# Performance work log

Hardware: AMD Instinct MI355X
Metric: run time of the kernel (lower is better)

The kernel has to match this reference:

```python
import jax, jax.numpy as jnp
import numpy as np

N_NODES = 100000
N_REL = 8
N_EDGES = 1_600_000
ED = 64   # entity_dim
RD = 64   # relation_dim
H = 4     # attention heads
A = 16    # attention dim per head
D1, D2 = 32, 16  # conv_dim_list


def _leaky(x):
    return jax.nn.leaky_relu(x, 0.01)  # nn.LeakyReLU default slope


def _l2norm(x):
    n = jnp.sqrt(jnp.sum(x * x, axis=1, keepdims=True))
    return x / jnp.maximum(n, 1e-12)  # F.normalize(p=2, dim=1)


def setup_inputs() -> dict:
    key = jax.random.key(0)
    ks = jax.random.split(key, 16)
    s = 0.1
    return dict(
        src=jax.random.randint(ks[0], (N_EDGES,), 0, N_NODES),
        dst=jax.random.randint(ks[1], (N_EDGES,), 0, N_NODES),
        etype=jax.random.randint(ks[2], (N_EDGES,), 0, N_REL),
        node_ids=jnp.arange(N_NODES),
        user_ids=jax.random.randint(ks[3], (1000,), 0, N_NODES),
        item_ids=jax.random.randint(ks[4], (4096,), 0, N_NODES),
        entity_embed=jax.random.normal(ks[5], (N_NODES, ED)) * s,
        rel_embed=jax.random.normal(ks[6], (N_REL, RD)) * s,
        W_R=jax.random.normal(ks[7], (N_REL, ED, RD)) * s,
        W_A=jax.random.normal(ks[8], (RD, H, A)) * s,
        W1_0=jax.random.normal(ks[9], (ED, D1 // H)) * s,
        b1_0=jnp.zeros((D1 // H,)),
        W2_0=jax.random.normal(ks[10], (ED, D1 // H)) * s,
        b2_0=jnp.zeros((D1 // H,)),
        W1_1=jax.random.normal(ks[11], (D1, D2 // H)) * s,
        b1_1=jnp.zeros((D2 // H,)),
        W2_1=jax.random.normal(ks[12], (D1, D2 // H)) * s,
        b2_1=jnp.zeros((D2 // H,)),
    )


def _compute_attention(entity_embed, rel_embed, W_R, W_A, src, dst, etype):
    # relation-specific edge attention: tanh(e_src W_r W_A) * tanh(e_dst W_r W_A + r W_A)
    WA_flat = W_A.reshape(RD, H * A)
    W_ra = jnp.einsum('rij,jk->rik', W_R, WA_flat)          # [R, ED, H*A]
    proj = jnp.einsum('ne,rek->rnk', entity_embed, W_ra)    # [R, N, H*A]
    r_emb_a = rel_embed @ WA_flat                           # [R, H*A]
    r_mul_t = jnp.tanh(proj[etype, src])                    # [E, H*A]
    r_mul_h = jnp.tanh(proj[etype, dst] + r_emb_a[etype])   # [E, H*A]
    att = (r_mul_t * r_mul_h).reshape(-1, H, A).sum(-1)     # [E, H]
    # edge softmax over incoming edges of each dst node, per head
    m = jax.ops.segment_max(att, dst, num_segments=N_NODES)
    m = jnp.where(jnp.isfinite(m), m, 0.0)
    e = jnp.exp(att - m[dst])
    z = jax.ops.segment_sum(e, dst, num_segments=N_NODES)
    return e / jnp.maximum(z[dst], 1e-12)                   # [E, H]


def _bi_layer(ego, att, src, dst, W1, b1, W2, b2, out_dim):
    # u_mul_e + sum: message = node[src] (broadcast over heads) * att[:, :, None]
    in_dim = ego.shape[1]
    msg = ego[src][:, None, :] * att[:, :, None]            # [E, H, in]
    N_h = jax.ops.segment_sum(msg, dst, num_segments=N_NODES)  # [N, H, in]
    node = ego[:, None, :]                                  # [N, 1, in]
    out1 = _leaky((node + N_h).reshape(-1, in_dim) @ W1 + b1).reshape(N_NODES, out_dim)
    out2 = _leaky((node * N_h).reshape(-1, in_dim) @ W2 + b2).reshape(N_NODES, out_dim)
    return out1 + out2  # dropout p=0 (eval)


def reference(src, dst, etype, node_ids, user_ids, item_ids,
              entity_embed, rel_embed, W_R, W_A,
              W1_0, b1_0, W2_0, b2_0, W1_1, b1_1, W2_1, b2_1):
    att = _compute_attention(entity_embed, rel_embed, W_R, W_A, src, dst, etype)
    ego = entity_embed[node_ids]
    ego1 = _bi_layer(ego, att, src, dst, W1_0, b1_0, W2_0, b2_0, D1)
    ego2 = _bi_layer(ego1, att, src, dst, W1_1, b1_1, W2_1, b2_1, D2)
    all_embed = jnp.concatenate([ego, _l2norm(ego1), _l2norm(ego2)], axis=1)  # [N, 112]
    return all_embed[user_ids] @ all_embed[item_ids].T     # [1000, 4096]
```

## Files before the change

kernel.cpp:

```cpp
#include <hip/hip_runtime.h>
#include <hip/hip_bf16.h>
#include <math.h>

#define NN 100000
#define NR 8
#define NE 1600000

typedef __attribute__((ext_vector_type(8))) short short8v;
typedef __attribute__((ext_vector_type(4))) float float4v;
typedef __attribute__((ext_vector_type(2))) float float2v;

__device__ inline float bf2f(unsigned short u) {
  union { unsigned int i; float f; } v; v.i = ((unsigned int)u) << 16; return v.f;
}
__device__ inline unsigned short f2bf(float f) {
  __hip_bfloat16 h = __float2bfloat16(f);
  return *reinterpret_cast<unsigned short*>(&h);
}
__device__ inline float fast_tanh(float x) {
  float ex = __expf(2.f * x);
  return 1.f - 2.f * __builtin_amdgcn_rcpf(ex + 1.f);
}
__device__ inline unsigned char f2fp8(float f) {
  unsigned int p = __builtin_amdgcn_cvt_pk_fp8_f32(f, f, 0, false);
  return (unsigned char)(p & 0xff);
}

__global__ void k_prep(const float* __restrict__ W_R, const float* __restrict__ W_A,
                       const float* __restrict__ rel, unsigned short* __restrict__ Wbf,
                       float* __restrict__ r_emb_a) {
  int tid = blockIdx.x * 256 + threadIdx.x;
  if (tid < NR * 64 * 64) {
    int r = tid >> 12;
    int i = (tid >> 6) & 63;
    int k = tid & 63;
    float acc = 0.f;
    const float* wr = W_R + (r * 64 + i) * 64;
    for (int j = 0; j < 64; ++j) acc += wr[j] * W_A[j * 64 + k];
    Wbf[(r * 64 + k) * 64 + i] = f2bf(acc);
  } else if (tid < NR * 64 * 64 + NR * 64) {
    int idx = tid - NR * 64 * 64;
    int r = idx >> 6, k = idx & 63;
    float acc = 0.f;
    for (int j = 0; j < 64; ++j) acc += rel[r * 64 + j] * W_A[j * 64 + k];
    r_emb_a[idx] = acc;
  }
}

__global__ void k_cvt(const float* __restrict__ E, unsigned short* __restrict__ Ebf) {
  int i = blockIdx.x * 256 + threadIdx.x;
  float4 v = ((const float4*)E)[i];
  ushort4 o;
  o.x = f2bf(v.x); o.y = f2bf(v.y); o.z = f2bf(v.z); o.w = f2bf(v.w);
  ((ushort4*)Ebf)[i] = o;
}

__global__ void k_proj(const unsigned short* __restrict__ Ebf,
                       const unsigned short* __restrict__ Wbf,
                       const float* __restrict__ rea,
                       unsigned char* __restrict__ T1, unsigned char* __restrict__ T2) {
  int wv = threadIdx.x >> 6, lane = threadIdx.x & 63;
  int n0 = blockIdx.x * 64 + wv * 16;
  int mrow = lane & 15, kg = lane >> 4;
  int nodeA = n0 + mrow;
  if (nodeA >= NN) nodeA = NN - 1;
  const short8v a0 = *(const short8v*)(Ebf + (long)nodeA * 64 + kg * 8);
  const short8v a1 = *(const short8v*)(Ebf + (long)nodeA * 64 + 32 + kg * 8);
  int orow = kg * 4;
  for (int ct = 0; ct < 32; ++ct) {
    int c = ct * 16 + mrow;
    const short8v b0 = *(const short8v*)(Wbf + c * 64 + kg * 8);
    const short8v b1 = *(const short8v*)(Wbf + c * 64 + 32 + kg * 8);
    float4v acc = {0.f, 0.f, 0.f, 0.f};
    acc = __builtin_amdgcn_mfma_f32_16x16x32_bf16(a0, b0, acc, 0, 0, 0);
    acc = __builtin_amdgcn_mfma_f32_16x16x32_bf16(a1, b1, acc, 0, 0, 0);
    float rv = rea[c];
    int r = c >> 6, kk = c & 63;
#pragma unroll
    for (int i = 0; i < 4; ++i) {
      int nd = n0 + orow + i;
      if (nd < NN) {
        long base = ((long)r * NN + nd) * 64 + kk;
        T1[base] = f2fp8(fast_tanh(acc[i]));
        T2[base] = f2fp8(fast_tanh(acc[i] + rv));
      }
    }
  }
}

__global__ void k_hist(const int* __restrict__ dst, int* __restrict__ cnt) {
  int e = blockIdx.x * 256 + threadIdx.x;
  if (e < NE) atomicAdd(&cnt[dst[e]], 1);
}

#define SCAN_B 1024
#define NSCAN ((NN + SCAN_B - 1) / SCAN_B)

__global__ void k_scan1(const int* __restrict__ cnt, int* __restrict__ rowp,
                        int* __restrict__ bsum) {
  __shared__ int s[SCAN_B];
  int t = threadIdx.x, g = blockIdx.x * SCAN_B + t;
  s[t] = (g < NN) ? cnt[g] : 0;
  __syncthreads();
  for (int off = 1; off < SCAN_B; off <<= 1) {
    int x = (t >= off) ? s[t - off] : 0;
    __syncthreads();
    s[t] += x;
    __syncthreads();
  }
  if (g < NN) rowp[g + 1] = s[t];
  if (t == SCAN_B - 1) bsum[blockIdx.x] = s[t];
}

__global__ void k_scan2(int* bsum) {
  if (threadIdx.x == 0) {
    int acc = 0;
    for (int i = 0; i < NSCAN; ++i) { int v = bsum[i]; bsum[i] = acc; acc += v; }
  }
}

__global__ void k_scan3(int* rowp, const int* __restrict__ bsum) {
  int t = threadIdx.x, g = blockIdx.x * SCAN_B + t;
  if (g < NN) rowp[g + 1] += bsum[blockIdx.x];
  if (g == 0) rowp[0] = 0;
}

__global__ void k_scatter(const int* __restrict__ src, const int* __restrict__ dst,
                          const int* __restrict__ etype, const int* __restrict__ rowp,
                          int* __restrict__ cur, uint2* __restrict__ rec) {
  int e = blockIdx.x * 256 + threadIdx.x;
  if (e >= NE) return;
  int d = dst[e];
  int p = rowp[d] + atomicAdd(&cur[d], 1);
  uint2 rv;
  rv.x = ((unsigned int)src[e] << 3) | (unsigned int)etype[e];
  rv.y = (unsigned int)d;
  rec[p] = rv;
}

__global__ void k_att(const unsigned char* __restrict__ T1,
                      const unsigned char* __restrict__ T2,
                      const uint2* __restrict__ rec, int* __restrict__ srcs,
                      float* __restrict__ att) {
  int gid = blockIdx.x * 256 + threadIdx.x;
  int e = gid >> 2;
  int h = gid & 3;
  if (e >= NE) return;
  uint2 rv = rec[e];
  int r = rv.x & 7;
  int s = rv.x >> 3;
  int d = (int)rv.y;
  const uint4 av = *(const uint4*)(T1 + ((long)r * NN + s) * 64 + h * 16);
  const uint4 bv = *(const uint4*)(T2 + ((long)r * NN + d) * 64 + h * 16);
  const unsigned int* ap = (const unsigned int*)&av;
  const unsigned int* bp = (const unsigned int*)&bv;
  float acc = 0.f;
#pragma unroll
  for (int i = 0; i < 4; ++i) {
    float2v a0 = __builtin_amdgcn_cvt_pk_f32_fp8(ap[i], false);
    float2v a1 = __builtin_amdgcn_cvt_pk_f32_fp8(ap[i], true);
    float2v b0 = __builtin_amdgcn_cvt_pk_f32_fp8(bp[i], false);
    float2v b1 = __builtin_amdgcn_cvt_pk_f32_fp8(bp[i], true);
    acc += a0.x * b0.x + a0.y * b0.y + a1.x * b1.x + a1.y * b1.y;
  }
  att[gid] = acc;
  if (h == 0) srcs[e] = s;
}

__global__ void k_softmax(const int* __restrict__ rowp, float* __restrict__ att) {
  int n = (blockIdx.x * 256 + threadIdx.x) >> 6;
  int lane = threadIdx.x & 63;
  if (n >= NN) return;
  int i0 = rowp[n] * 4, i1 = rowp[n + 1] * 4;
  float m = -3.4e38f;
  for (int i = i0 + lane; i < i1; i += 64) m = fmaxf(m, att[i]);
  m = fmaxf(m, __shfl_xor(m, 4));
  m = fmaxf(m, __shfl_xor(m, 8));
  m = fmaxf(m, __shfl_xor(m, 16));
  m = fmaxf(m, __shfl_xor(m, 32));
  float z = 0.f;
  for (int i = i0 + lane; i < i1; i += 64) z += __expf(att[i] - m);
  z += __shfl_xor(z, 4);
  z += __shfl_xor(z, 8);
  z += __shfl_xor(z, 16);
  z += __shfl_xor(z, 32);
  float inv = 1.f / fmaxf(z, 1e-12f);
  for (int i = i0 + lane; i < i1; i += 64) att[i] = __expf(att[i] - m) * inv;
}

__global__ void k_fused0(const float* __restrict__ E, const unsigned short* __restrict__ Ebf,
                         const float* __restrict__ attn,
                         const int* __restrict__ rowp, const int* __restrict__ srcs,
                         const float* __restrict__ W1, const float* __restrict__ b1,
                         const float* __restrict__ W2, const float* __restrict__ b2,
                         float* __restrict__ ego1, unsigned short* __restrict__ ego1bf) {
  __shared__ float wt1[8][68], wt2[8][68];
  __shared__ float bb[16];
  __shared__ float s1[4][4][68], s2[4][4][68];
  int t = threadIdx.x;
  for (int i = t; i < 512; i += 256) {
    int d = i >> 3, j = i & 7;
    wt1[j][d] = W1[i];
    wt2[j][d] = W2[i];
  }
  if (t < 8) bb[t] = b1[t];
  else if (t < 16) bb[t] = b2[t - 8];
  __syncthreads();
  int wv = t >> 6, lane = t & 63;
  int n = blockIdx.x * 4 + wv;
  int p0 = rowp[n], p1 = rowp[n + 1];
  int g = lane >> 4, q = lane & 15;
  float acc[4][4];
#pragma unroll
  for (int h = 0; h < 4; ++h)
#pragma unroll
    for (int j = 0; j < 4; ++j) acc[h][j] = 0.f;
  for (int p = p0 + g; p < p1; p += 4) {
    int s = srcs[p];
    float4 a = ((const float4*)attn)[p];
    ushort4 ev = *(const ushort4*)(Ebf + s * 64 + q * 4);
    float e0 = bf2f(ev.x), e1 = bf2f(ev.y), e2 = bf2f(ev.z), e3 = bf2f(ev.w);
    acc[0][0] += a.x * e0; acc[0][1] += a.x * e1; acc[0][2] += a.x * e2; acc[0][3] += a.x * e3;
    acc[1][0] += a.y * e0; acc[1][1] += a.y * e1; acc[1][2] += a.y * e2; acc[1][3] += a.y * e3;
    acc[2][0] += a.z * e0; acc[2][1] += a.z * e1; acc[2][2] += a.z * e2; acc[2][3] += a.z * e3;
    acc[3][0] += a.w * e0; acc[3][1] += a.w * e1; acc[3][2] += a.w * e2; acc[3][3] += a.w * e3;
  }
#pragma unroll
  for (int h = 0; h < 4; ++h)
#pragma unroll
    for (int j = 0; j < 4; ++j) {
      acc[h][j] += __shfl_xor(acc[h][j], 16);
      acc[h][j] += __shfl_xor(acc[h][j], 32);
    }
  if (lane < 16) {
    float4 edv = *(const float4*)(E + n * 64 + q * 4);
#pragma unroll
    for (int h = 0; h < 4; ++h) {
      float4 v1, v2;
      v1.x = edv.x + acc[h][0]; v2.x = edv.x * acc[h][0];
      v1.y = edv.y + acc[h][1]; v2.y = edv.y * acc[h][1];
      v1.z = edv.z + acc[h][2]; v2.z = edv.z * acc[h][2];
      v1.w = edv.w + acc[h][3]; v2.w = edv.w * acc[h][3];
      *(float4*)&s1[wv][h][q * 4] = v1;
      *(float4*)&s2[wv][h][q * 4] = v2;
    }
  }
  __syncthreads();
  int h = (lane >> 3) & 3, j = lane & 7;
  const float* sp = (lane < 32) ? &s1[wv][h][0] : &s2[wv][h][0];
  const float* wp = (lane < 32) ? &wt1[j][0] : &wt2[j][0];
  float o = 0.f;
#pragma unroll
  for (int d = 0; d < 64; d += 4) {
    float4 sv = *(const float4*)(sp + d);
    float4 wv4 = *(const float4*)(wp + d);
    o += sv.x * wv4.x + sv.y * wv4.y + sv.z * wv4.z + sv.w * wv4.w;
  }
  o += (lane < 32) ? bb[j] : bb[8 + j];
  o = (o >= 0.f) ? o : 0.01f * o;
  float other = __shfl_xor(o, 32);
  if (lane < 32) {
    float r = o + other;
    ego1[n * 32 + h * 8 + j] = r;
    ego1bf[n * 32 + h * 8 + j] = f2bf(r);
  }
}

__global__ void k_fused1(const float* __restrict__ ego1, const unsigned short* __restrict__ E1bf,
                         const float* __restrict__ attn,
                         const int* __restrict__ rowp, const int* __restrict__ srcs,
                         const float* __restrict__ W1, const float* __restrict__ b1,
                         const float* __restrict__ W2, const float* __restrict__ b2,
                         float* __restrict__ ego2) {
  __shared__ float wt1[4][36], wt2[4][36], bb[8];
  __shared__ float s1[4][4][36], s2[4][4][36];
  int t = threadIdx.x;
  if (t < 128) { int d = t >> 2, j = t & 3; wt1[j][d] = W1[t]; wt2[j][d] = W2[t]; }
  if (t < 4) bb[t] = b1[t];
  else if (t < 8) bb[t] = b2[t - 4];
  __syncthreads();
  int wv = t >> 6, lane = t & 63;
  int n = blockIdx.x * 4 + wv;
  int p0 = rowp[n], p1 = rowp[n + 1];
  int g = lane >> 3, q = lane & 7;
  float acc[4][4];
#pragma unroll
  for (int h = 0; h < 4; ++h)
#pragma unroll
    for (int j = 0; j < 4; ++j) acc[h][j] = 0.f;
  for (int p = p0 + g; p < p1; p += 8) {
    int s = srcs[p];
    float4 a = ((const float4*)attn)[p];
    ushort4 ev = *(const ushort4*)(E1bf + s * 32 + q * 4);
    float e0 = bf2f(ev.x), e1 = bf2f(ev.y), e2 = bf2f(ev.z), e3 = bf2f(ev.w);
    acc[0][0] += a.x * e0; acc[0][1] += a.x * e1; acc[0][2] += a.x * e2; acc[0][3] += a.x * e3;
    acc[1][0] += a.y * e0; acc[1][1] += a.y * e1; acc[1][2] += a.y * e2; acc[1][3] += a.y * e3;
    acc[2][0] += a.z * e0; acc[2][1] += a.z * e1; acc[2][2] += a.z * e2; acc[2][3] += a.z * e3;
    acc[3][0] += a.w * e0; acc[3][1] += a.w * e1; acc[3][2] += a.w * e2; acc[3][3] += a.w * e3;
  }
#pragma unroll
  for (int h = 0; h < 4; ++h)
#pragma unroll
    for (int j = 0; j < 4; ++j) {
      acc[h][j] += __shfl_xor(acc[h][j], 8);
      acc[h][j] += __shfl_xor(acc[h][j], 16);
      acc[h][j] += __shfl_xor(acc[h][j], 32);
    }
  if (lane < 8) {
    float4 e1v = *(const float4*)(ego1 + n * 32 + q * 4);
#pragma unroll
    for (int h = 0; h < 4; ++h) {
      float4 v1, v2;
      v1.x = e1v.x + acc[h][0]; v2.x = e1v.x * acc[h][0];
      v1.y = e1v.y + acc[h][1]; v2.y = e1v.y * acc[h][1];
      v1.z = e1v.z + acc[h][2]; v2.z = e1v.z * acc[h][2];
      v1.w = e1v.w + acc[h][3]; v2.w = e1v.w * acc[h][3];
      *(float4*)&s1[wv][h][q * 4] = v1;
      *(float4*)&s2[wv][h][q * 4] = v2;
    }
  }
  __syncthreads();
  if (lane < 32) {
    int h = (lane >> 2) & 3, j = lane & 3;
    const float* sp = (lane < 16) ? &s1[wv][h][0] : &s2[wv][h][0];
    const float* wp = (lane < 16) ? &wt1[j][0] : &wt2[j][0];
    float o = 0.f;
#pragma unroll
    for (int d = 0; d < 32; d += 4) {
      float4 sv = *(const float4*)(sp + d);
      float4 wv4 = *(const float4*)(wp + d);
      o += sv.x * wv4.x + sv.y * wv4.y + sv.z * wv4.z + sv.w * wv4.w;
    }
    o += (lane < 16) ? bb[j] : bb[4 + j];
    o = (o >= 0.f) ? o : 0.01f * o;
    float other = __shfl_xor(o, 16);
    if (lane < 16) ego2[n * 16 + h * 4 + j] = o + other;
  }
}

__global__ void k_uv(const float* __restrict__ E, const float* __restrict__ E1,
                     const float* __restrict__ E2, const int* __restrict__ uid,
                     const int* __restrict__ iid, float* __restrict__ U,
                     float* __restrict__ V) {
  int row = (blockIdx.x * 256 + threadIdx.x) >> 6;
  int lane = threadIdx.x & 63;
  if (row >= 1000 + 4096) return;
  int id = (row < 1000) ? uid[row] : iid[row - 1000];
  float* dest = (row < 1000) ? (U + row * 112) : (V + (row - 1000) * 112);
  float v1 = (lane < 32) ? E1[id * 32 + lane] : 0.f;
  float s1 = v1 * v1;
  for (int m = 1; m < 64; m <<= 1) s1 += __shfl_xor(s1, m);
  float v2 = (lane < 16) ? E2[id * 16 + lane] : 0.f;
  float s2 = v2 * v2;
  for (int m = 1; m < 64; m <<= 1) s2 += __shfl_xor(s2, m);
  float i1 = 1.f / fmaxf(sqrtf(s1), 1e-12f);
  float i2 = 1.f / fmaxf(sqrtf(s2), 1e-12f);
  dest[lane] = E[id * 64 + lane];
  if (lane < 32) dest[64 + lane] = v1 * i1;
  if (lane < 16) dest[96 + lane] = v2 * i2;
}

__global__ void k_gemm(const float* __restrict__ U, const float* __restrict__ V,
                       float* __restrict__ C) {
  __shared__ float Us[16][113], Vs[16][113];
  int tx = threadIdx.x & 15, ty = threadIdx.x >> 4;
  int u0 = blockIdx.y * 16, v0 = blockIdx.x * 16;
  for (int i = threadIdx.x; i < 16 * 112; i += 256) {
    int rr = i / 112, cc = i % 112;
    int ur = u0 + rr;
    Us[rr][cc] = (ur < 1000) ? U[ur * 112 + cc] : 0.f;
    Vs[rr][cc] = V[(v0 + rr) * 112 + cc];
  }
  __syncthreads();
  int u = u0 + ty;
  if (u >= 1000) return;
  float acc = 0.f;
#pragma unroll
  for (int k = 0; k < 112; ++k) acc += Us[ty][k] * Vs[tx][k];
  C[u * 4096 + v0 + tx] = acc;
}

extern "C" void kernel_launch(void* const* d_in, const int* in_sizes, int n_in,
                              void* d_out, int out_size, void* d_ws, size_t ws_size,
                              hipStream_t stream) {
  const int* src = (const int*)d_in[0];
  const int* dst = (const int*)d_in[1];
  const int* etype = (const int*)d_in[2];
  const int* uid = (const int*)d_in[4];
  const int* iid = (const int*)d_in[5];
  const float* entity = (const float*)d_in[6];
  const float* rel = (const float*)d_in[7];
  const float* W_R = (const float*)d_in[8];
  const float* W_A = (const float*)d_in[9];
  const float* W1_0 = (const float*)d_in[10];
  const float* b1_0 = (const float*)d_in[11];
  const float* W2_0 = (const float*)d_in[12];
  const float* b2_0 = (const float*)d_in[13];
  const float* W1_1 = (const float*)d_in[14];
  const float* b1_1 = (const float*)d_in[15];
  const float* W2_1 = (const float*)d_in[16];
  const float* b2_1 = (const float*)d_in[17];
  float* out = (float*)d_out;

  char* ws = (char*)d_ws;
  unsigned char*  T1   = (unsigned char*) (ws + 0);
  float*          ego1 = (float*)         (ws + 0);
  unsigned short* e1bf = (unsigned short*)(ws + 12800000);
  float*          ego2 = (float*)         (ws + 19200000);
  float*          U    = (float*)         (ws + 25600000);
  float*          V    = (float*)         (ws + 26048000);
  unsigned char*  T2   = (unsigned char*) (ws + 51200000);
  float*          att  = (float*)         (ws + 102400000);
  uint2*          rec  = (uint2*)         (ws + 128000000);
  int*            srcs = (int*)           (ws + 140800000);
  int*            rowp = (int*)           (ws + 147200000);
  int*            cnt  = (int*)           (ws + 147600128);
  int*            bsum = (int*)           (ws + 148000256);
  unsigned short* Wbf  = (unsigned short*)(ws + 148000768);
  float*          rea  = (float*)         (ws + 148066304);
  unsigned short* Ebf  = (unsigned short*)(ws + 148068352);

  hipMemsetAsync(cnt, 0, NN * sizeof(int), stream);
  k_prep<<<130, 256, 0, stream>>>(W_R, W_A, rel, Wbf, rea);
  k_cvt<<<6250, 256, 0, stream>>>(entity, Ebf);
  k_proj<<<(NN + 63) / 64, 256, 0, stream>>>(Ebf, Wbf, rea, T1, T2);
  k_hist<<<NE / 256, 256, 0, stream>>>(dst, cnt);
  k_scan1<<<NSCAN, SCAN_B, 0, stream>>>(cnt, rowp, bsum);
  k_scan2<<<1, 64, 0, stream>>>(bsum);
  k_scan3<<<NSCAN, SCAN_B, 0, stream>>>(rowp, bsum);
  hipMemsetAsync(cnt, 0, NN * sizeof(int), stream);
  k_scatter<<<NE / 256, 256, 0, stream>>>(src, dst, etype, rowp, cnt, rec);
  k_att<<<NE * 4 / 256, 256, 0, stream>>>(T1, T2, rec, srcs, att);
  k_softmax<<<NN / 4, 256, 0, stream>>>(rowp, att);
  k_fused0<<<NN / 4, 256, 0, stream>>>(entity, Ebf, att, rowp, srcs,
                                       W1_0, b1_0, W2_0, b2_0, ego1, e1bf);
  k_fused1<<<NN / 4, 256, 0, stream>>>(ego1, e1bf, att, rowp, srcs,
                                       W1_1, b1_1, W2_1, b2_1, ego2);
  k_uv<<<(1000 + 4096 + 3) / 4, 256, 0, stream>>>(entity, ego1, ego2, uid, iid, U, V);
  k_gemm<<<dim3(4096 / 16, (1000 + 15) / 16), 256, 0, stream>>>(U, V, out);
}
```

Measured before the change: 610.2 us.

## Fuse edge attention and softmax into layer-0 aggregation with node-major projections

Removes the separate attention and softmax kernels by computing per-edge attention scores inside k_fused0. It uses unnormalized exp weights and applies the per-head reciprocal sum at the end. The projection tables are relaid out node-major ([N][512]) so that one wave reads a contiguous 64-byte row per edge. Edge records shrink to 4 bytes, and layer 1 reuses the stored exp weights with the saved normalizers. Dropping the max subtraction risks overflow for large scores. The layer-0 loop now handles edges one at a time with shuffle reductions, which serializes work per node.

New measurement: 695.0 us. 1.14x slower.

```diff
diff --git a/kernel.cpp b/kernel.cpp
--- a/kernel.cpp
+++ b/kernel.cpp
@@ -24,6 +24,10 @@
 __device__ inline unsigned char f2fp8(float f) {
   unsigned int p = __builtin_amdgcn_cvt_pk_fp8_f32(f, f, 0, false);
   return (unsigned char)(p & 0xff);
+}
+__device__ inline float fp82f(unsigned char b) {
+  float2v v = __builtin_amdgcn_cvt_pk_f32_fp8((unsigned int)b, false);
+  return v.x;
 }
 
 __global__ void k_prep(const float* __restrict__ W_R, const float* __restrict__ W_A,
@@ -58,7 +62,7 @@
 __global__ void k_proj(const unsigned short* __restrict__ Ebf,
                        const unsigned short* __restrict__ Wbf,
                        const float* __restrict__ rea,
-                       unsigned char* __restrict__ T1, unsigned char* __restrict__ T2) {
+                       unsigned char* __restrict__ T1n, unsigned char* __restrict__ T2n) {
   int wv = threadIdx.x >> 6, lane = threadIdx.x & 63;
   int n0 = blockIdx.x * 64 + wv * 16;
   int mrow = lane & 15, kg = lane >> 4;
@@ -75,14 +79,13 @@
     acc = __builtin_amdgcn_mfma_f32_16x16x32_bf16(a0, b0, acc, 0, 0, 0);
     acc = __builtin_amdgcn_mfma_f32_16x16x32_bf16(a1, b1, acc, 0, 0, 0);
     float rv = rea[c];
-    int r = c >> 6, kk = c & 63;
 #pragma unroll
     for (int i = 0; i < 4; ++i) {
       int nd = n0 + orow + i;
       if (nd < NN) {
-        long base = ((long)r * NN + nd) * 64 + kk;
-        T1[base] = f2fp8(fast_tanh(acc[i]));
-        T2[base] = f2fp8(fast_tanh(acc[i] + rv));
+        long base = (long)nd * 512 + c;
+        T1n[base] = f2fp8(fast_tanh(acc[i]));
+        T2n[base] = f2fp8(fast_tanh(acc[i] + rv));
       }
     }
   }
@@ -127,70 +130,20 @@
 
 __global__ void k_scatter(const int* __restrict__ src, const int* __restrict__ dst,
                           const int* __restrict__ etype, const int* __restrict__ rowp,
-                          int* __restrict__ cur, uint2* __restrict__ rec) {
+                          int* __restrict__ cur, unsigned int* __restrict__ rec) {
   int e = blockIdx.x * 256 + threadIdx.x;
   if (e >= NE) return;
   int d = dst[e];
   int p = rowp[d] + atomicAdd(&cur[d], 1);
-  uint2 rv;
-  rv.x = ((unsigned int)src[e] << 3) | (unsigned int)etype[e];
-  rv.y = (unsigned int)d;
-  rec[p] = rv;
-}
-
-__global__ void k_att(const unsigned char* __restrict__ T1,
-                      const unsigned char* __restrict__ T2,
-                      const uint2* __restrict__ rec, int* __restrict__ srcs,
-                      float* __restrict__ att) {
-  int gid = blockIdx.x * 256 + threadIdx.x;
-  int e = gid >> 2;
-  int h = gid & 3;
-  if (e >= NE) return;
-  uint2 rv = rec[e];
-  int r = rv.x & 7;
-  int s = rv.x >> 3;
-  int d = (int)rv.y;
-  const uint4 av = *(const uint4*)(T1 + ((long)r * NN + s) * 64 + h * 16);
-  const uint4 bv = *(const uint4*)(T2 + ((long)r * NN + d) * 64 + h * 16);
-  const unsigned int* ap = (const unsigned int*)&av;
-  const unsigned int* bp = (const unsigned int*)&bv;
-  float acc = 0.f;
-#pragma unroll
-  for (int i = 0; i < 4; ++i) {
-    float2v a0 = __builtin_amdgcn_cvt_pk_f32_fp8(ap[i], false);
-    float2v a1 = __builtin_amdgcn_cvt_pk_f32_fp8(ap[i], true);
-    float2v b0 = __builtin_amdgcn_cvt_pk_f32_fp8(bp[i], false);
-    float2v b1 = __builtin_amdgcn_cvt_pk_f32_fp8(bp[i], true);
-    acc += a0.x * b0.x + a0.y * b0.y + a1.x * b1.x + a1.y * b1.y;
-  }
-  att[gid] = acc;
-  if (h == 0) srcs[e] = s;
-}
-
-__global__ void k_softmax(const int* __restrict__ rowp, float* __restrict__ att) {
-  int n = (blockIdx.x * 256 + threadIdx.x) >> 6;
-  int lane = threadIdx.x & 63;
-  if (n >= NN) return;
-  int i0 = rowp[n] * 4, i1 = rowp[n + 1] * 4;
-  float m = -3.4e38f;
-  for (int i = i0 + lane; i < i1; i += 64) m = fmaxf(m, att[i]);
-  m = fmaxf(m, __shfl_xor(m, 4));
-  m = fmaxf(m, __shfl_xor(m, 8));
-  m = fmaxf(m, __shfl_xor(m, 16));
-  m = fmaxf(m, __shfl_xor(m, 32));
-  float z = 0.f;
-  for (int i = i0 + lane; i < i1; i += 64) z += __expf(att[i] - m);
-  z += __shfl_xor(z, 4);
-  z += __shfl_xor(z, 8);
-  z += __shfl_xor(z, 16);
-  z += __shfl_xor(z, 32);
-  float inv = 1.f / fmaxf(z, 1e-12f);
-  for (int i = i0 + lane; i < i1; i += 64) att[i] = __expf(att[i] - m) * inv;
+  rec[p] = ((unsigned int)src[e] << 3) | (unsigned int)etype[e];
 }
 
 __global__ void k_fused0(const float* __restrict__ E, const unsigned short* __restrict__ Ebf,
-                         const float* __restrict__ attn,
-                         const int* __restrict__ rowp, const int* __restrict__ srcs,
+                         const unsigned char* __restrict__ T1n,
+                         const unsigned char* __restrict__ T2n,
+                         const unsigned int* __restrict__ rec,
+                         const int* __restrict__ rowp,
+                         float* __restrict__ att4, float* __restrict__ zinv4,
                          const float* __restrict__ W1, const float* __restrict__ b1,
                          const float* __restrict__ W2, const float* __restrict__ b2,
                          float* __restrict__ ego1, unsigned short* __restrict__ ego1bf) {
@@ -209,42 +162,51 @@
   int wv = t >> 6, lane = t & 63;
   int n = blockIdx.x * 4 + wv;
   int p0 = rowp[n], p1 = rowp[n + 1];
-  int g = lane >> 4, q = lane & 15;
-  float acc[4][4];
-#pragma unroll
-  for (int h = 0; h < 4; ++h)
-#pragma unroll
-    for (int j = 0; j < 4; ++j) acc[h][j] = 0.f;
-  for (int p = p0 + g; p < p1; p += 4) {
-    int s = srcs[p];
-    float4 a = ((const float4*)attn)[p];
-    ushort4 ev = *(const ushort4*)(Ebf + s * 64 + q * 4);
-    float e0 = bf2f(ev.x), e1 = bf2f(ev.y), e2 = bf2f(ev.z), e3 = bf2f(ev.w);
-    acc[0][0] += a.x * e0; acc[0][1] += a.x * e1; acc[0][2] += a.x * e2; acc[0][3] += a.x * e3;
-    acc[1][0] += a.y * e0; acc[1][1] += a.y * e1; acc[1][2] += a.y * e2; acc[1][3] += a.y * e3;
-    acc[2][0] += a.z * e0; acc[2][1] += a.z * e1; acc[2][2] += a.z * e2; acc[2][3] += a.z * e3;
-    acc[3][0] += a.w * e0; acc[3][1] += a.w * e1; acc[3][2] += a.w * e2; acc[3][3] += a.w * e3;
-  }
-#pragma unroll
-  for (int h = 0; h < 4; ++h)
-#pragma unroll
-    for (int j = 0; j < 4; ++j) {
-      acc[h][j] += __shfl_xor(acc[h][j], 16);
-      acc[h][j] += __shfl_xor(acc[h][j], 32);
-    }
-  if (lane < 16) {
-    float4 edv = *(const float4*)(E + n * 64 + q * 4);
-#pragma unroll
-    for (int h = 0; h < 4; ++h) {
-      float4 v1, v2;
-      v1.x = edv.x + acc[h][0]; v2.x = edv.x * acc[h][0];
-      v1.y = edv.y + acc[h][1]; v2.y = edv.y * acc[h][1];
-      v1.z = edv.z + acc[h][2]; v2.z = edv.z * acc[h][2];
-      v1.w = edv.w + acc[h][3]; v2.w = edv.w * acc[h][3];
-      *(float4*)&s1[wv][h][q * 4] = v1;
-      *(float4*)&s2[wv][h][q * 4] = v2;
-    }
-  }
+  int head = lane >> 4, base = lane & 15;
+  float acc0 = 0.f, acc1 = 0.f, acc2 = 0.f, acc3 = 0.f, z = 0.f;
+  if (p0 < p1) {
+    unsigned int rv = rec[p0];
+    int s = rv >> 3, r = rv & 7;
+    unsigned char a8 = T1n[(long)s * 512 + r * 64 + lane];
+    unsigned char b8 = T2n[(long)n * 512 + r * 64 + lane];
+    unsigned short ev16 = Ebf[s * 64 + lane];
+    for (int p = p0; p < p1; ++p) {
+      int pn = (p + 1 < p1) ? p + 1 : p;
+      unsigned int rvn = rec[pn];
+      int sn = rvn >> 3, rn = rvn & 7;
+      unsigned char a8n = T1n[(long)sn * 512 + rn * 64 + lane];
+      unsigned char b8n = T2n[(long)n * 512 + rn * 64 + lane];
+      unsigned short evn = Ebf[sn * 64 + lane];
+      float a = fp82f(a8), b = fp82f(b8);
+      float prod = a * b;
+      prod += __shfl_xor(prod, 1);
+      prod += __shfl_xor(prod, 2);
+      prod += __shfl_xor(prod, 4);
+      prod += __shfl_xor(prod, 8);
+      float e = __expf(prod);
+      z += e;
+      float w0 = __shfl(e, base);
+      float w1 = __shfl(e, 16 + base);
+      float w2 = __shfl(e, 32 + base);
+      float w3 = __shfl(e, 48 + base);
+      if (lane == 0) ((float4*)att4)[p] = make_float4(w0, w1, w2, w3);
+      float ev = bf2f(ev16);
+      acc0 += w0 * ev; acc1 += w1 * ev; acc2 += w2 * ev; acc3 += w3 * ev;
+      a8 = a8n; b8 = b8n; ev16 = evn;
+    }
+  }
+  float zi = 1.f / fmaxf(z, 1e-12f);
+  if (base == 0) zinv4[n * 4 + head] = zi;
+  float zi0 = __shfl(zi, base);
+  float zi1 = __shfl(zi, 16 + base);
+  float zi2 = __shfl(zi, 32 + base);
+  float zi3 = __shfl(zi, 48 + base);
+  acc0 *= zi0; acc1 *= zi1; acc2 *= zi2; acc3 *= zi3;
+  float ed = E[n * 64 + lane];
+  s1[wv][0][lane] = ed + acc0; s2[wv][0][lane] = ed * acc0;
+  s1[wv][1][lane] = ed + acc1; s2[wv][1][lane] = ed * acc1;
+  s1[wv][2][lane] = ed + acc2; s2[wv][2][lane] = ed * acc2;
+  s1[wv][3][lane] = ed + acc3; s2[wv][3][lane] = ed * acc3;
   __syncthreads();
   int h = (lane >> 3) & 3, j = lane & 7;
   const float* sp = (lane < 32) ? &s1[wv][h][0] : &s2[wv][h][0];
@@ -267,8 +229,9 @@
 }
 
 __global__ void k_fused1(const float* __restrict__ ego1, const unsigned short* __restrict__ E1bf,
-                         const float* __restrict__ attn,
-                         const int* __restrict__ rowp, const int* __restrict__ srcs,
+                         const float* __restrict__ att4, const float* __restrict__ zinv4,
+                         const unsigned int* __restrict__ rec,
+                         const int* __restrict__ rowp,
                          const float* __restrict__ W1, const float* __restrict__ b1,
                          const float* __restrict__ W2, const float* __restrict__ b2,
                          float* __restrict__ ego2) {
@@ -289,8 +252,8 @@
 #pragma unroll
     for (int j = 0; j < 4; ++j) acc[h][j] = 0.f;
   for (int p = p0 + g; p < p1; p += 8) {
-    int s = srcs[p];
-    float4 a = ((const float4*)attn)[p];
+    int s = (int)(rec[p] >> 3);
+    float4 a = ((const float4*)att4)[p];
     ushort4 ev = *(const ushort4*)(E1bf + s * 32 + q * 4);
     float e0 = bf2f(ev.x), e1 = bf2f(ev.y), e2 = bf2f(ev.z), e3 = bf2f(ev.w);
     acc[0][0] += a.x * e0; acc[0][1] += a.x * e1; acc[0][2] += a.x * e2; acc[0][3] += a.x * e3;
@@ -307,6 +270,11 @@
       acc[h][j] += __shfl_xor(acc[h][j], 32);
     }
   if (lane < 8) {
+    float4 zi = *(const float4*)(zinv4 + n * 4);
+#pragma unroll
+    for (int j = 0; j < 4; ++j) {
+      acc[0][j] *= zi.x; acc[1][j] *= zi.y; acc[2][j] *= zi.z; acc[3][j] *= zi.w;
+    }
     float4 e1v = *(const float4*)(ego1 + n * 32 + q * 4);
 #pragma unroll
     for (int h = 0; h < 4; ++h) {
@@ -403,38 +371,37 @@
   float* out = (float*)d_out;
 
   char* ws = (char*)d_ws;
-  unsigned char*  T1   = (unsigned char*) (ws + 0);
-  float*          ego1 = (float*)         (ws + 0);
-  unsigned short* e1bf = (unsigned short*)(ws + 12800000);
-  float*          ego2 = (float*)         (ws + 19200000);
-  float*          U    = (float*)         (ws + 25600000);
-  float*          V    = (float*)         (ws + 26048000);
-  unsigned char*  T2   = (unsigned char*) (ws + 51200000);
-  float*          att  = (float*)         (ws + 102400000);
-  uint2*          rec  = (uint2*)         (ws + 128000000);
-  int*            srcs = (int*)           (ws + 140800000);
-  int*            rowp = (int*)           (ws + 147200000);
-  int*            cnt  = (int*)           (ws + 147600128);
-  int*            bsum = (int*)           (ws + 148000256);
-  unsigned short* Wbf  = (unsigned short*)(ws + 148000768);
-  float*          rea  = (float*)         (ws + 148066304);
-  unsigned short* Ebf  = (unsigned short*)(ws + 148068352);
+  unsigned char*  T1n  = (unsigned char*) (ws + 0);
+  unsigned char*  T2n  = (unsigned char*) (ws + 51200000);
+  float*          att4 = (float*)         (ws + 102400000);
+  unsigned int*   rec  = (unsigned int*)  (ws + 128000000);
+  int*            rowp = (int*)           (ws + 134400000);
+  int*            cnt  = (int*)           (ws + 134800128);
+  int*            bsum = (int*)           (ws + 135200256);
+  unsigned short* Wbf  = (unsigned short*)(ws + 135200768);
+  float*          rea  = (float*)         (ws + 135266304);
+  unsigned short* Ebf  = (unsigned short*)(ws + 135268352);
+  float*          zinv4= (float*)         (ws + 148068352);
+  float*          ego1 = (float*)         (ws + 149668352);
+  unsigned short* e1bf = (unsigned short*)(ws + 162468352);
+  float*          ego2 = (float*)         (ws + 168868352);
+  float*          U    = (float*)         (ws + 175268352);
+  float*          V    = (float*)         (ws + 175716352);
 
   hipMemsetAsync(cnt, 0, NN * sizeof(int), stream);
   k_prep<<<130, 256, 0, stream>>>(W_R, W_A, rel, Wbf, rea);
   k_cvt<<<6250, 256, 0, stream>>>(entity, Ebf);
-  k_proj<<<(NN + 63) / 64, 256, 0, stream>>>(Ebf, Wbf, rea, T1, T2);
+  k_proj<<<(NN + 63) / 64, 256, 0, stream>>>(Ebf, Wbf, rea, T1n, T2n);
   k_hist<<<NE / 256, 256, 0, stream>>>(dst, cnt);
   k_scan1<<<NSCAN, SCAN_B, 0, stream>>>(cnt, rowp, bsum);
   k_scan2<<<1, 64, 0, stream>>>(bsum);
   k_scan3<<<NSCAN, SCAN_B, 0, stream>>>(rowp, bsum);
   hipMemsetAsync(cnt, 0, NN * sizeof(int), stream);
   k_scatter<<<NE / 256, 256, 0, stream>>>(src, dst, etype, rowp, cnt, rec);
-  k_att<<<NE * 4 / 256, 256, 0, stream>>>(T1, T2, rec, srcs, att);
-  k_softmax<<<NN / 4, 256, 0, stream>>>(rowp, att);
-  k_fused0<<<NN / 4, 256, 0, stream>>>(entity, Ebf, att, rowp, srcs,
-                                       W1_0, b1_0, W2_0, b2_0, ego1, e1bf);
-  k_fused1<<<NN / 4, 256, 0, stream>>>(ego1, e1bf, att, rowp, srcs,
+  k_fused0<<<NN / 4, 256, 0, stream>>>(entity, Ebf, T1n, T2n, rec, rowp,
+                                       att4, zinv4, W1_0, b1_0, W2_0, b2_0,
+                                       ego1, e1bf);
+  k_fused1<<<NN / 4, 256, 0, stream>>>(ego1, e1bf, att4, zinv4, rec, rowp,
                                        W1_1, b1_1, W2_1, b2_1, ego2);
   k_uv<<<(1000 + 4096 + 3) / 4, 256, 0, stream>>>(entity, ego1, ego2, uid, iid, U, V);
   k_gemm<<<dim3(4096 / 16, (1000 + 15) / 16), 256, 0, stream>>>(U, V, out);
```
